# Kernel tuning notes

Hardware: AMD Instinct MI355X
Metric: run time of the kernel (lower is better)

The kernel has to match this reference:

```python
import jax, jax.numpy as jnp
import numpy as np

K = 512
D = 256


def setup_inputs() -> dict:
    key = jax.random.key(0)
    k1, k2 = jax.random.split(key)
    x = jax.random.normal(k1, (64, D, 32, 32), dtype=jnp.float32)
    # nn.Embedding(K, D) init: uniform(-1/K, 1/K)
    emb = jax.random.uniform(k2, (K, D), dtype=jnp.float32, minval=-1.0 / K, maxval=1.0 / K)
    return {"x": x, "emb": emb}


def reference(x, emb):
    # encoder is identity: z_e_x = x, shape [B, D, H, W]
    B, Dd, H, W = x.shape
    z_e = jnp.transpose(x, (0, 2, 3, 1))           # [B, H, W, D]
    z_flat = z_e.reshape(-1, Dd)                    # [N, D]
    # squared euclidean distances to codebook: ||z||^2 + ||e||^2 - 2 z.e
    dist = (jnp.sum(z_flat * z_flat, axis=1, keepdims=True)
            + jnp.sum(emb * emb, axis=1)[None, :]
            - 2.0 * z_flat @ emb.T)                 # [N, K]
    idx = jnp.argmin(dist, axis=1)                  # [N]
    codes = emb[idx]                                # [N, D] gather
    codes = codes.reshape(B, H, W, Dd)
    # straight-through quantized output (value == codes)
    z_q_st = z_e + jax.lax.stop_gradient(codes - z_e)
    z_q_st = jnp.transpose(z_q_st, (0, 3, 1, 2))    # [B, D, H, W]
    # z_q_x_bar: gathered from live codebook (grads flow to emb)
    z_q_bar = jnp.transpose(codes, (0, 3, 1, 2))    # [B, D, H, W]
    # decoder is identity: x_tilde = z_q_st
    return (z_q_st, x, z_q_bar)
```

## Files before the change

### kernel.cpp

```cpp
#include <hip/hip_runtime.h>


#define B_  64
#define D_  256
#define HW_ 1024
#define K_  512

typedef __attribute__((ext_vector_type(8))) short short8;
typedef __attribute__((ext_vector_type(4))) float f32x4;

__device__ unsigned short g_ebf[K_ * D_];
__device__ float g_e2[K_];
__device__ float g_embT[D_ * K_];
__device__ int   g_idx[B_ * HW_];

__device__ __forceinline__ unsigned short f2bf(float f) {
    unsigned u = __float_as_uint(f);
    u += 0x7fffu + ((u >> 16) & 1u);
    return (unsigned short)(u >> 16);
}

__global__ void prep(const float* __restrict__ emb) {
    const int t   = threadIdx.x;
    const int row = blockIdx.x * 8 + (t >> 5);
    const int c0  = (t & 31) * 8;
    const float* rp = emb + row * D_ + c0;
    float4 a = *(const float4*)rp;
    float4 b = *(const float4*)(rp + 4);
    short8 v;
    v[0] = (short)f2bf(a.x); v[1] = (short)f2bf(a.y);
    v[2] = (short)f2bf(a.z); v[3] = (short)f2bf(a.w);
    v[4] = (short)f2bf(b.x); v[5] = (short)f2bf(b.y);
    v[6] = (short)f2bf(b.z); v[7] = (short)f2bf(b.w);
    *(short8*)(g_ebf + row * D_ + c0) = v;
    g_embT[(c0 + 0) * K_ + row] = a.x;
    g_embT[(c0 + 1) * K_ + row] = a.y;
    g_embT[(c0 + 2) * K_ + row] = a.z;
    g_embT[(c0 + 3) * K_ + row] = a.w;
    g_embT[(c0 + 4) * K_ + row] = b.x;
    g_embT[(c0 + 5) * K_ + row] = b.y;
    g_embT[(c0 + 6) * K_ + row] = b.z;
    g_embT[(c0 + 7) * K_ + row] = b.w;
    float ps = a.x*a.x + a.y*a.y + a.z*a.z + a.w*a.w
             + b.x*b.x + b.y*b.y + b.z*b.z + b.w*b.w;
    ps += __shfl_xor(ps, 1);  ps += __shfl_xor(ps, 2);
    ps += __shfl_xor(ps, 4);  ps += __shfl_xor(ps, 8);
    ps += __shfl_xor(ps, 16);
    if ((t & 31) == 0) g_e2[row] = ps;
}

__global__ __launch_bounds__(256, 4)
void vq_argmin(const float* __restrict__ x) {
    __shared__ unsigned short cb[2][32 * 256];

    const int t   = threadIdx.x;
    const int w   = t >> 6;
    const int l   = t & 63;
    const int blk = blockIdx.x;
    const int b   = blk >> 4;
    const int hw0 = (blk & 15) << 6;
    const float* xb = x + ((size_t)b * D_) * HW_ + hw0;

    short8 zb[8];
    float* xt = (float*)&cb[0][0];
    for (int R = 0; R < 4; ++R) {
#pragma unroll
        for (int k2 = 0; k2 < 4; ++k2) {
            const int k  = 4 * w + k2;
            const int dr = 4 * k + (l >> 4);
            const float* gp = xb + (size_t)(64 * R + dr) * HW_ + (l & 15) * 4;
            float* lp = xt + 256 * k;
            __builtin_amdgcn_global_load_lds(
                (const __attribute__((address_space(1))) unsigned int*)gp,
                (__attribute__((address_space(3))) unsigned int*)lp, 16, 0, 0);
        }
        __syncthreads();
#pragma unroll
        for (int h = 0; h < 2; ++h) {
            short8 f;
#pragma unroll
            for (int j = 0; j < 8; ++j) {
                const int dl = h * 32 + (l >> 4) * 8 + j;
                f[j] = (short)f2bf(xt[dl * 64 + 16 * w + (l & 15)]);
            }
            zb[2 * R + h] = f;
        }
        __syncthreads();
    }

#define STAGEC(cc, bb) do {                                                   \
        _Pragma("unroll")                                                     \
        for (int k2 = 0; k2 < 4; ++k2) {                                      \
            const int k  = 4 * w + k2;                                        \
            const int rl = 2 * k + (l >> 5);        \
            const unsigned short* gp = g_ebf + ((cc) * 32 + rl) * 256         \
                                       + (((l & 31) ^ (rl & 7)) << 3);        \
            unsigned short* lp = &cb[bb][512 * k];                            \
            __builtin_amdgcn_global_load_lds(                                 \
                (const __attribute__((address_space(1))) unsigned int*)gp,    \
                (__attribute__((address_space(3))) unsigned int*)lp, 16, 0, 0);\
        }                                                                     \
    } while (0)

    float minv = 3.0e38f;
    int   mini = 0;

    STAGEC(0, 0);
    __syncthreads();
    for (int c = 0; c < 16; ++c) {
        if (c + 1 < 16) STAGEC(c + 1, (c + 1) & 1);
        const unsigned short* cbuf = cb[c & 1];
#pragma unroll
        for (int ct2 = 0; ct2 < 2; ++ct2) {
            f32x4 acc = {0.f, 0.f, 0.f, 0.f};
            const int cr = ct2 * 16 + (l & 15);
#pragma unroll
            for (int s = 0; s < 8; ++s) {
                const int unit = ((l >> 4) + 4 * s) ^ (cr & 7);
                short8 a = *(const short8*)(cbuf + cr * 256 + unit * 8);
                acc = __builtin_amdgcn_mfma_f32_16x16x32_bf16(a, zb[s], acc, 0, 0, 0);
            }
            const int cbase = 32 * c + 16 * ct2 + (l >> 4) * 4;
            f32x4 e2v = *(const f32x4*)(g_e2 + cbase);
#pragma unroll
            for (int r = 0; r < 4; ++r) {
                const float sv = e2v[r] - 2.0f * acc[r];
                if (sv < minv) { minv = sv; mini = cbase + r; }
            }
        }
        __syncthreads();
    }

    {
        float ov; int oi;
        ov = __shfl_xor(minv, 16); oi = __shfl_xor(mini, 16);
        if (ov < minv || (ov == minv && oi < mini)) { minv = ov; mini = oi; }
        ov = __shfl_xor(minv, 32); oi = __shfl_xor(mini, 32);
        if (ov < minv || (ov == minv && oi < mini)) { minv = ov; mini = oi; }
    }
    if (l < 16) g_idx[b * HW_ + hw0 + 16 * w + l] = mini;
}

__global__ __launch_bounds__(256)
void vq_scatter(const float* __restrict__ x, float* __restrict__ out0,
                float* __restrict__ out1, float* __restrict__ out2) {
    __shared__ float et[8 * 512];
    const int t   = threadIdx.x;
    const int blk = blockIdx.x;
    const int b   = blk >> 5;
    const int d0  = (blk & 31) << 3;
    {
        const float4* src = (const float4*)(g_embT + (size_t)d0 * K_);
        float4* dst = (float4*)et;
#pragma unroll
        for (int i = 0; i < 4; ++i) dst[t + 256 * i] = src[t + 256 * i];
    }
    const int4 mi = *(const int4*)(g_idx + b * HW_ + 4 * t);
    __syncthreads();
    const size_t base = ((size_t)b * D_ + d0) * HW_ + 4 * t;
    const float* xp = x + base;
    float* p0 = out0 + base;
    float* p1 = out1 + base;
    float* p2 = out2 + base;
#pragma unroll
    for (int r = 0; r < 8; ++r) {
        const float* er = et + r * 512;
        const size_t off = (size_t)r * HW_;
        f32x4 xv = *(const f32x4*)(xp + off);
        f32x4 cv;
        cv[0] = er[mi.x]; cv[1] = er[mi.y];
        cv[2] = er[mi.z]; cv[3] = er[mi.w];
        __builtin_nontemporal_store(xv, (f32x4*)(p1 + off));
        __builtin_nontemporal_store(cv, (f32x4*)(p0 + off));
        __builtin_nontemporal_store(cv, (f32x4*)(p2 + off));
    }
}

extern "C" void kernel_launch(void* const* d_in, const int* in_sizes, int n_in,
                              void* d_out, int out_size, void* d_ws, size_t ws_size,
                              hipStream_t stream) {
    const float* x   = (const float*)d_in[0];
    const float* emb = (const float*)d_in[1];
    float* out0 = (float*)d_out;
    float* out1 = out0 + (size_t)16777216;
    float* out2 = out0 + (size_t)33554432;

    prep<<<64, 256, 0, stream>>>(emb);
    vq_argmin<<<1024, 256, 0, stream>>>(x);
    vq_scatter<<<2048, 256, 0, stream>>>(x, out0, out1, out2);
}
```

Baseline: 273.7 us.

## Write x copy from argmin kernel LDS tile; double pixels per block

The argmin kernel now processes 128 pixels per block (two MFMA accumulators sharing each codebook fragment) and writes the x passthrough output directly from the staged LDS tile. The scatter kernel no longer re-reads x or writes out1. This removes a second full read of x and halves how often the codebook is restaged per pixel. In exchange the grid shrinks to 512 blocks, each with more registers, and the argmin kernel takes on 64MB of stores.

```diff
diff --git a/kernel.cpp b/kernel.cpp
--- a/kernel.cpp
+++ b/kernel.cpp
@@ -50,25 +50,26 @@
 }
 
 __global__ __launch_bounds__(256, 4)
-void vq_argmin(const float* __restrict__ x) {
+void vq_argmin(const float* __restrict__ x, float* __restrict__ out1) {
     __shared__ unsigned short cb[2][32 * 256];
 
     const int t   = threadIdx.x;
     const int w   = t >> 6;
     const int l   = t & 63;
     const int blk = blockIdx.x;
-    const int b   = blk >> 4;
-    const int hw0 = (blk & 15) << 6;
-    const float* xb = x + ((size_t)b * D_) * HW_ + hw0;
-
-    short8 zb[8];
+    const int b   = blk >> 3;
+    const int hw0 = (blk & 7) << 7;
+    const float* xb = x    + ((size_t)b * D_) * HW_ + hw0;
+    float*       o1 = out1 + ((size_t)b * D_) * HW_ + hw0;
+
+    short8 zb[2][8];
     float* xt = (float*)&cb[0][0];
     for (int R = 0; R < 4; ++R) {
 #pragma unroll
-        for (int k2 = 0; k2 < 4; ++k2) {
-            const int k  = 4 * w + k2;
-            const int dr = 4 * k + (l >> 4);
-            const float* gp = xb + (size_t)(64 * R + dr) * HW_ + (l & 15) * 4;
+        for (int k2 = 0; k2 < 8; ++k2) {
+            const int k  = 8 * w + k2;
+            const int dr = 2 * k + (l >> 5);
+            const float* gp = xb + (size_t)(64 * R + dr) * HW_ + (l & 31) * 4;
             float* lp = xt + 256 * k;
             __builtin_amdgcn_global_load_lds(
                 (const __attribute__((address_space(1))) unsigned int*)gp,
@@ -77,13 +78,26 @@
         __syncthreads();
 #pragma unroll
         for (int h = 0; h < 2; ++h) {
-            short8 f;
-#pragma unroll
-            for (int j = 0; j < 8; ++j) {
-                const int dl = h * 32 + (l >> 4) * 8 + j;
-                f[j] = (short)f2bf(xt[dl * 64 + 16 * w + (l & 15)]);
-            }
-            zb[2 * R + h] = f;
+#pragma unroll
+            for (int pt = 0; pt < 2; ++pt) {
+                short8 f;
+#pragma unroll
+                for (int j = 0; j < 8; ++j) {
+                    const int dl = 32 * h + (l >> 4) * 8 + j;
+                    f[j] = (short)f2bf(xt[dl * 128 + 32 * w + 16 * pt + (l & 15)]);
+                }
+                zb[pt][2 * R + h] = f;
+            }
+        }
+#pragma unroll
+        for (int rr = 0; rr < 16; ++rr) {
+            const int dl = 16 * w + rr;
+            const size_t gro = (size_t)(64 * R + dl) * HW_;
+#pragma unroll
+            for (int h2 = 0; h2 < 2; ++h2) {
+                const float vv = xt[dl * 128 + 64 * h2 + l];
+                __builtin_nontemporal_store(vv, o1 + gro + 64 * h2 + l);
+            }
         }
         __syncthreads();
     }
@@ -102,8 +116,8 @@
         }                                                                     \
     } while (0)
 
-    float minv = 3.0e38f;
-    int   mini = 0;
+    float minv0 = 3.0e38f, minv1 = 3.0e38f;
+    int   mini0 = 0,       mini1 = 0;
 
     STAGEC(0, 0);
     __syncthreads();
@@ -112,20 +126,23 @@
         const unsigned short* cbuf = cb[c & 1];
 #pragma unroll
         for (int ct2 = 0; ct2 < 2; ++ct2) {
-            f32x4 acc = {0.f, 0.f, 0.f, 0.f};
+            f32x4 a0 = {0.f, 0.f, 0.f, 0.f}, a1 = {0.f, 0.f, 0.f, 0.f};
             const int cr = ct2 * 16 + (l & 15);
 #pragma unroll
             for (int s = 0; s < 8; ++s) {
                 const int unit = ((l >> 4) + 4 * s) ^ (cr & 7);
                 short8 a = *(const short8*)(cbuf + cr * 256 + unit * 8);
-                acc = __builtin_amdgcn_mfma_f32_16x16x32_bf16(a, zb[s], acc, 0, 0, 0);
+                a0 = __builtin_amdgcn_mfma_f32_16x16x32_bf16(a, zb[0][s], a0, 0, 0, 0);
+                a1 = __builtin_amdgcn_mfma_f32_16x16x32_bf16(a, zb[1][s], a1, 0, 0, 0);
             }
             const int cbase = 32 * c + 16 * ct2 + (l >> 4) * 4;
             f32x4 e2v = *(const f32x4*)(g_e2 + cbase);
 #pragma unroll
             for (int r = 0; r < 4; ++r) {
-                const float sv = e2v[r] - 2.0f * acc[r];
-                if (sv < minv) { minv = sv; mini = cbase + r; }
+                const float s0 = e2v[r] - 2.0f * a0[r];
+                const float s1 = e2v[r] - 2.0f * a1[r];
+                if (s0 < minv0) { minv0 = s0; mini0 = cbase + r; }
+                if (s1 < minv1) { minv1 = s1; mini1 = cbase + r; }
             }
         }
         __syncthreads();
@@ -133,17 +150,23 @@
 
     {
         float ov; int oi;
-        ov = __shfl_xor(minv, 16); oi = __shfl_xor(mini, 16);
-        if (ov < minv || (ov == minv && oi < mini)) { minv = ov; mini = oi; }
-        ov = __shfl_xor(minv, 32); oi = __shfl_xor(mini, 32);
-        if (ov < minv || (ov == minv && oi < mini)) { minv = ov; mini = oi; }
-    }
-    if (l < 16) g_idx[b * HW_ + hw0 + 16 * w + l] = mini;
+        ov = __shfl_xor(minv0, 16); oi = __shfl_xor(mini0, 16);
+        if (ov < minv0 || (ov == minv0 && oi < mini0)) { minv0 = ov; mini0 = oi; }
+        ov = __shfl_xor(minv0, 32); oi = __shfl_xor(mini0, 32);
+        if (ov < minv0 || (ov == minv0 && oi < mini0)) { minv0 = ov; mini0 = oi; }
+        ov = __shfl_xor(minv1, 16); oi = __shfl_xor(mini1, 16);
+        if (ov < minv1 || (ov == minv1 && oi < mini1)) { minv1 = ov; mini1 = oi; }
+        ov = __shfl_xor(minv1, 32); oi = __shfl_xor(mini1, 32);
+        if (ov < minv1 || (ov == minv1 && oi < mini1)) { minv1 = ov; mini1 = oi; }
+    }
+    if (l < 16) {
+        g_idx[b * HW_ + hw0 + 32 * w + l]      = mini0;
+        g_idx[b * HW_ + hw0 + 32 * w + 16 + l] = mini1;
+    }
 }
 
 __global__ __launch_bounds__(256)
-void vq_scatter(const float* __restrict__ x, float* __restrict__ out0,
-                float* __restrict__ out1, float* __restrict__ out2) {
+void vq_scatter(float* __restrict__ out0, float* __restrict__ out2) {
     __shared__ float et[8 * 512];
     const int t   = threadIdx.x;
     const int blk = blockIdx.x;
@@ -158,19 +181,15 @@
     const int4 mi = *(const int4*)(g_idx + b * HW_ + 4 * t);
     __syncthreads();
     const size_t base = ((size_t)b * D_ + d0) * HW_ + 4 * t;
-    const float* xp = x + base;
     float* p0 = out0 + base;
-    float* p1 = out1 + base;
     float* p2 = out2 + base;
 #pragma unroll
     for (int r = 0; r < 8; ++r) {
         const float* er = et + r * 512;
         const size_t off = (size_t)r * HW_;
-        f32x4 xv = *(const f32x4*)(xp + off);
         f32x4 cv;
         cv[0] = er[mi.x]; cv[1] = er[mi.y];
         cv[2] = er[mi.z]; cv[3] = er[mi.w];
-        __builtin_nontemporal_store(xv, (f32x4*)(p1 + off));
         __builtin_nontemporal_store(cv, (f32x4*)(p0 + off));
         __builtin_nontemporal_store(cv, (f32x4*)(p2 + off));
     }
@@ -186,6 +205,6 @@
     float* out2 = out0 + (size_t)33554432;
 
     prep<<<64, 256, 0, stream>>>(emb);
-    vq_argmin<<<1024, 256, 0, stream>>>(x);
-    vq_scatter<<<2048, 256, 0, stream>>>(x, out0, out1, out2);
-}
+    vq_argmin<<<512, 256, 0, stream>>>(x, out1);
+    vq_scatter<<<2048, 256, 0, stream>>>(out0, out2);
+}
```

Result: slower. 295.6 us (+8.0%).
